# Performance work log

Hardware: AMD Instinct MI355X
Metric: run time of the kernel (lower is better)

The kernel has to match this reference:

```python
import jax, jax.numpy as jnp
import numpy as np

N = 10000   # nodes
E = 50000   # edges
G = 8       # graphs in batch
IN = 16     # input_dim
H = 64      # hidden_dim
EH = 32     # edge-network hidden
L = 3       # num ECC layers
BN_EPS = 1e-5


def _xavier(k, shape):
    fan_in, fan_out = shape[-2], shape[-1]
    s = jnp.sqrt(2.0 / (fan_in + fan_out)).astype(jnp.float32)
    return jax.random.normal(k, shape, jnp.float32) * s


def setup_inputs() -> dict:
    key = jax.random.key(0)
    ks = jax.random.split(key, 10)
    x = jax.random.normal(ks[0], (N, IN), jnp.float32)
    edge_index = jax.random.randint(ks[1], (2, E), 0, N, jnp.int32)
    batch = jnp.sort(jax.random.randint(ks[2], (N,), 0, G, jnp.int32))
    return {
        "x": x,
        "edge_index": edge_index,
        "batch": batch,
        "emb_w": _xavier(ks[3], (IN, H)),
        "emb_b": jnp.zeros((H,), jnp.float32),
        "e1_w": _xavier(ks[4], (L, 1, EH)),
        "e1_b": jnp.zeros((L, EH), jnp.float32),
        "e2_w": _xavier(ks[5], (L, EH, H * H)),
        "e2_b": jnp.zeros((L, H * H), jnp.float32),
        "self_w": _xavier(ks[6], (L, H, H)),
        "self_b": jnp.zeros((L, H), jnp.float32),
        "bn_g": jnp.ones((L, H), jnp.float32),
        "bn_b": jnp.zeros((L, H), jnp.float32),
        "cls_w": _xavier(ks[7], (2 * H, 1)),
        "cls_b": jnp.zeros((1,), jnp.float32),
    }


def reference(x, edge_index, batch, emb_w, emb_b, e1_w, e1_b, e2_w, e2_b,
              self_w, self_b, bn_g, bn_b, cls_w, cls_b):
    src, dst = edge_index[0], edge_index[1]
    # in-degree of targets for 'mean' aggregation (computed once; edge structure fixed)
    deg = jnp.clip(jax.ops.segment_sum(jnp.ones((E,), x.dtype), dst, num_segments=N), 1.0, None)

    h = x @ emb_w + emb_b  # [N, H] input embedding
    for l in range(L):
        # edge_attr: L2 distance between first 3 hidden channels of endpoints, [E,1]
        d = h[src, :3] - h[dst, :3]
        ea = jnp.sqrt(jnp.sum(d * d, axis=1, keepdims=True))
        # edge network -> per-edge dynamic weight matrix [E, H, H]
        hid = jax.nn.relu(ea @ e1_w[l] + e1_b[l])          # [E, EH]
        W = (hid @ e2_w[l] + e2_b[l]).reshape(E, H, H)
        # message: x_j (source features) times per-edge weight
        msg = jnp.einsum('ei,eio->eo', h[src], W)          # [E, H]
        agg = jax.ops.segment_sum(msg, dst, num_segments=N) / deg[:, None]
        h2 = agg + h @ self_w[l] + self_b[l]               # ECC output + self transform
        # BatchNorm1d (training-mode batch stats, biased variance), then ReLU
        mu = h2.mean(axis=0)
        var = h2.var(axis=0)
        h = jax.nn.relu(bn_g[l] * (h2 - mu) * jax.lax.rsqrt(var + BN_EPS) + bn_b[l])
        # dropout is a no-op in eval mode

    cnt = jnp.clip(jax.ops.segment_sum(jnp.ones((N,), h.dtype), batch, num_segments=G), 1.0, None)
    h_mean = jax.ops.segment_sum(h, batch, num_segments=G) / cnt[:, None]
    h_max = jax.ops.segment_max(h, batch, num_segments=G)
    h_pooled = jnp.concatenate([h_mean, h_max], axis=1)    # [G, 2H]
    return jax.nn.sigmoid(h_pooled @ cls_w + cls_b)        # [G, 1]
```

## Files before the change

### kernel.cpp

```cpp
#include <hip/hip_runtime.h>
#include <math.h>

#define N_NODES 10000
#define N_EDGES 50000
#define N_GRAPHS 8
#define IN_DIM  16
#define HID     64
#define EHID    32
#define NLAYER  3
#define NK      33
#define BN_EPS  1e-5f
#define POOL_BLOCKS 63
#define LAYER_BLOCKS 625
#define MAXDEG  64

#define FB_EMBED 2500
#define FB_S2    (16 * NK * NLAYER)
#define FB_AUX   3
#define FB_TOTAL (FB_EMBED + FB_S2 + FB_AUX)

#define OFF_H0     0u
#define OFF_H2A    640000u
#define OFF_H2B    1280000u
#define OFF_ATAB   1920000u
#define OFF_CTAB   2325504u
#define OFF_S      2731008u
#define OFF_NB     2731136u
#define OFF_CUR    2731200u
#define OFF_CSRC   2741200u
#define OFF_STATS  3381200u
#define OFF_GSUM   3381584u
#define OFF_GMAX   3382096u
#define OFF_GCNT   3382608u
#define OFF_CNTR   3382616u

__device__ __forceinline__ float rl(float v, int i) {
    return __int_as_float(__builtin_amdgcn_readlane(__float_as_int(v), i));
}

__device__ __forceinline__ void bn_coef(const float* __restrict__ sPrev,
                                        const float* __restrict__ gPrev,
                                        const float* __restrict__ bPrev,
                                        int c, float& sc, float& sf) {
    float mu  = sPrev[c] * (1.0f / N_NODES);
    float var = fmaf(-mu, mu, sPrev[64 + c] * (1.0f / N_NODES));
    float rstd = 1.0f / sqrtf(var + BN_EPS);
    sc = gPrev[c] * rstd;
    sf = fmaf(-sc, mu, bPrev[c]);
}

__device__ __forceinline__ int bp_list(const float* __restrict__ e1w,
                                       const float* __restrict__ e1b,
                                       int l, float* t) {
    int c = 0;
    for (int j = 0; j < EHID; ++j) {
        float a = e1w[l * EHID + j], b = e1b[l * EHID + j];
        if ((a > 0.f && b < 0.f) || (a < 0.f && b > 0.f)) t[c++] = -b / a;
    }
    for (int i = 1; i < c; ++i) {
        float v = t[i]; int j = i - 1;
        while (j >= 0 && t[j] > v) { t[j + 1] = t[j]; --j; }
        t[j + 1] = v;
    }
    return c;
}

__global__ void k_front(const float* __restrict__ x, const float* __restrict__ emb_w,
                        const float* __restrict__ emb_b,
                        const float* __restrict__ e1w, const float* __restrict__ e1b,
                        const float* __restrict__ e2w, const float* __restrict__ e2b,
                        float* __restrict__ s_arr, int* __restrict__ nb,
                        int* __restrict__ cur, float* __restrict__ stats,
                        float* __restrict__ gsum, float* __restrict__ gmax,
                        int* __restrict__ gcnt, int* __restrict__ counter,
                        float* __restrict__ Atab, float* __restrict__ Ctab,
                        float* __restrict__ h0) {
    int b = blockIdx.x, tid = threadIdx.x;
    if (b < FB_EMBED) {
        int idx = b * 256 + tid;
        int n = idx >> 6, o = idx & 63;
        const float* xr = x + n * IN_DIM;
        float acc = emb_b[o];
        #pragma unroll
        for (int i = 0; i < IN_DIM; ++i) acc = fmaf(xr[i], emb_w[i * HID + o], acc);
        h0[idx] = acc;
    } else if (b < FB_EMBED + FB_S2) {
        __shared__ float st[EHID];
        __shared__ int snb;
        __shared__ float sma[EHID], smb[EHID];
        __shared__ float4 rA[4][64], rC[4][64];
        int job = b - FB_EMBED;
        int qq  = job / (NK * NLAYER);
        int rem = job % (NK * NLAYER);
        int k = rem / NLAYER, l = rem % NLAYER;
        if (tid == 0) {
            float t[EHID];
            int c = bp_list(e1w, e1b, l, t);
            snb = c;
            for (int i = 0; i < c; ++i) st[i] = t[i];
        }
        __syncthreads();
        int nbl = snb;
        if (k > nbl) return;
        if (tid < EHID) {
            float a = e1w[l * EHID + tid], bb = e1b[l * EHID + tid];
            float lo = (k == 0) ? 0.f : st[k - 1];
            float hi = st[k];
            float p  = (k == nbl) ? (lo + 1.0f) : 0.5f * (lo + hi);
            float m  = (p * a + bb > 0.f) ? 1.f : 0.f;
            sma[tid] = m * a;
            smb[tid] = m * bb;
        }
        __syncthreads();
        int lane6 = tid & 63, grp = tid >> 6;
        int f4 = qq * 64 + lane6;
        const float4* w4 = (const float4*)e2w;
        float4 accA = make_float4(0.f, 0.f, 0.f, 0.f);
        float4 accC = make_float4(0.f, 0.f, 0.f, 0.f);
        #pragma unroll
        for (int jj = 0; jj < 8; ++jj) {
            int j = grp * 8 + jj;
            float4 w = w4[(l * EHID + j) * 1024 + f4];
            float ma = sma[j], mb = smb[j];
            accA.x = fmaf(ma, w.x, accA.x); accA.y = fmaf(ma, w.y, accA.y);
            accA.z = fmaf(ma, w.z, accA.z); accA.w = fmaf(ma, w.w, accA.w);
            accC.x = fmaf(mb, w.x, accC.x); accC.y = fmaf(mb, w.y, accC.y);
            accC.z = fmaf(mb, w.z, accC.z); accC.w = fmaf(mb, w.w, accC.w);
        }
        rA[grp][lane6] = accA;
        rC[grp][lane6] = accC;
        __syncthreads();
        if (grp == 0) {
            float4 a0 = rA[0][lane6], a1 = rA[1][lane6], a2 = rA[2][lane6], a3 = rA[3][lane6];
            float4 c0 = rC[0][lane6], c1 = rC[1][lane6], c2 = rC[2][lane6], c3 = rC[3][lane6];
            float4 eb = ((const float4*)(e2b + l * HID * HID))[f4];
            float4 A, C;
            A.x = a0.x + a1.x + a2.x + a3.x; A.y = a0.y + a1.y + a2.y + a3.y;
            A.z = a0.z + a1.z + a2.z + a3.z; A.w = a0.w + a1.w + a2.w + a3.w;
            C.x = c0.x + c1.x + c2.x + c3.x + eb.x; C.y = c0.y + c1.y + c2.y + c3.y + eb.y;
            C.z = c0.z + c1.z + c2.z + c3.z + eb.z; C.w = c0.w + c1.w + c2.w + c3.w + eb.w;
            ((float4*)(Atab + (l * NK + k) * (HID * HID)))[f4] = A;
            ((float4*)(Ctab + (l * NK + k) * (HID * HID)))[f4] = C;
        }
    } else {
        int a = b - FB_EMBED - FB_S2;
        if (a == 0) {
            for (int i = tid; i < N_NODES; i += 256) cur[i] = 0;
        } else if (a == 1) {
            for (int i = tid; i < N_GRAPHS * HID; i += 256) { gsum[i] = 0.f; gmax[i] = 0.f; }
            if (tid < N_GRAPHS) gcnt[tid] = 0;
            if (tid == 0) *counter = 0;
        } else {
            for (int i = tid; i < NLAYER * 128; i += 256) stats[i] = 0.f;
            if (tid < NLAYER) {
                float t[EHID];
                int c = bp_list(e1w, e1b, tid, t);
                nb[tid] = c;
                for (int i = 0; i < c; ++i) s_arr[tid * NK + i] = t[i];
            }
        }
    }
}

__global__ void k_fill(const int* __restrict__ ei, int* __restrict__ cur,
                       int* __restrict__ csrc) {
    int e = blockIdx.x * blockDim.x + threadIdx.x;
    if (e < N_EDGES) {
        int dst = ei[N_EDGES + e];
        int pos = atomicAdd(&cur[dst], 1);
        if (pos < MAXDEG) csrc[dst * MAXDEG + pos] = ei[e];
    }
}

__global__ void __launch_bounds__(256, 3)
k_layer(const float* __restrict__ hb, int useBN,
        const float* __restrict__ sPrev, const float* __restrict__ gPrev,
        const float* __restrict__ bPrev,
        const int* __restrict__ csrc, const int* __restrict__ deg,
        const float* __restrict__ Atab, const float* __restrict__ Ctab,
        const float* __restrict__ s_arr, const int* __restrict__ nbp, int l,
        const float* __restrict__ sw_l, const float* __restrict__ sb_l,
        float* __restrict__ h2out, float* __restrict__ statsOut) {
    __shared__ float smW[3 * HID * HID];
    __shared__ float sRed[2][4][HID];
    int tid = threadIdx.x, wid = tid >> 6, lane = tid & 63;
    int nb = nbp[l];
    const float* A0 = Atab + l * NK * HID * HID;
    const float* C0 = Ctab + l * NK * HID * HID;
    {
        float4* s4 = (float4*)smW;
        const float4* w4 = (const float4*)sw_l;
        const float4* a4 = (const float4*)A0;
        const float4* c4 = (const float4*)C0;
        #pragma unroll
        for (int p = 0; p < 4; ++p) {
            int j = p * 256 + tid;
            s4[j] = w4[j];
            s4[1024 + j] = a4[j];
            s4[2048 + j] = c4[j];
        }
    }
    __syncthreads();
    float sc = 0.f, sf = 0.f;
    if (useBN) bn_coef(sPrev, gPrev, bPrev, lane, sc, sf);
    float sbv = sb_l[lane];
    int nodeBase = blockIdx.x * 16 + wid * 4;

    float hvv[4], pp[4], qq[4], aggE[4];
    #pragma unroll
    for (int c = 0; c < 4; ++c) {
        int node = nodeBase + c;
        float hv = hb[node * HID + lane];
        if (useBN) hv = fmaxf(fmaf(sc, hv, sf), 0.f);
        hvv[c] = hv;
        float p = 0.f, q = 0.f, aggv = 0.f;
        int cnt = min(deg[node], MAXDEG);
        const int base = node * MAXDEG;
        if (nb == 0) {
            int j = 0;
            for (; j + 4 <= cnt; j += 4) {
                int s0 = csrc[base + j],     s1 = csrc[base + j + 1];
                int s2 = csrc[base + j + 2], s3 = csrc[base + j + 3];
                float g0 = hb[s0 * HID + lane];
                float g1 = hb[s1 * HID + lane];
                float g2 = hb[s2 * HID + lane];
                float g3 = hb[s3 * HID + lane];
                #pragma unroll
                for (int u = 0; u < 4; ++u) {
                    float hs = (u == 0) ? g0 : (u == 1) ? g1 : (u == 2) ? g2 : g3;
                    if (useBN) hs = fmaxf(fmaf(sc, hs, sf), 0.f);
                    float diff = hs - hv;
                    float d0 = rl(diff, 0), d1 = rl(diff, 1), d2 = rl(diff, 2);
                    float ea = sqrtf(fmaf(d0, d0, fmaf(d1, d1, d2 * d2)));
                    p = fmaf(ea, hs, p);
                    q += hs;
                }
            }
            for (; j < cnt; ++j) {
                int s = csrc[base + j];
                float hs = hb[s * HID + lane];
                if (useBN) hs = fmaxf(fmaf(sc, hs, sf), 0.f);
                float diff = hs - hv;
                float d0 = rl(diff, 0), d1 = rl(diff, 1), d2 = rl(diff, 2);
                float ea = sqrtf(fmaf(d0, d0, fmaf(d1, d1, d2 * d2)));
                p = fmaf(ea, hs, p);
                q += hs;
            }
        } else {
            for (int j = 0; j < cnt; ++j) {
                int src = csrc[base + j];
                float hs = hb[src * HID + lane];
                if (useBN) hs = fmaxf(fmaf(sc, hs, sf), 0.f);
                float diff = hs - hv;
                float d0 = rl(diff, 0), d1 = rl(diff, 1), d2 = rl(diff, 2);
                float ea = sqrtf(fmaf(d0, d0, fmaf(d1, d1, d2 * d2)));
                int k = 0;
                for (int i = 0; i < nb; ++i) k += (ea > s_arr[l * NK + i]) ? 1 : 0;
                const float* A = Atab + (l * NK + k) * (HID * HID);
                const float* C = Ctab + (l * NK + k) * (HID * HID);
                float au = 0.f, cu = 0.f;
                for (int i = 0; i < HID; ++i) {
                    float hi = rl(hs, i);
                    au = fmaf(hi, A[i * HID + lane], au);
                    cu = fmaf(hi, C[i * HID + lane], cu);
                }
                aggv += fmaf(ea, au, cu);
            }
        }
        pp[c] = p; qq[c] = q; aggE[c] = aggv;
    }

    float acc[4], agg[4];
    #pragma unroll
    for (int c = 0; c < 4; ++c) { acc[c] = sbv; agg[c] = 0.f; }
    #pragma unroll
    for (int i = 0; i < HID; ++i) {
        float ws = smW[i * HID + lane];
        float wa = smW[HID * HID + i * HID + lane];
        float wc = smW[2 * HID * HID + i * HID + lane];
        #pragma unroll
        for (int c = 0; c < 4; ++c) {
            acc[c] = fmaf(rl(hvv[c], i), ws, acc[c]);
            agg[c] = fmaf(rl(pp[c], i), wa, agg[c]);
            agg[c] = fmaf(rl(qq[c], i), wc, agg[c]);
        }
    }

    float ls = 0.f, ls2 = 0.f;
    #pragma unroll
    for (int c = 0; c < 4; ++c) {
        int node = nodeBase + c;
        float invd = 1.0f / fmaxf((float)deg[node], 1.0f);
        float v = fmaf(agg[c] + aggE[c], invd, acc[c]);
        h2out[node * HID + lane] = v;
        ls += v; ls2 = fmaf(v, v, ls2);
    }
    sRed[0][wid][lane] = ls;
    sRed[1][wid][lane] = ls2;
    __syncthreads();
    if (tid < HID) {
        float s  = sRed[0][0][tid] + sRed[0][1][tid] + sRed[0][2][tid] + sRed[0][3][tid];
        float s2 = sRed[1][0][tid] + sRed[1][1][tid] + sRed[1][2][tid] + sRed[1][3][tid];
        atomicAdd(&statsOut[tid], s);
        atomicAdd(&statsOut[64 + tid], s2);
    }
}

__global__ void k_bnpool(const float* __restrict__ h2cur, const float* __restrict__ s2,
                         const float* __restrict__ g2, const float* __restrict__ b2,
                         const int* __restrict__ batch,
                         float* __restrict__ gsum, float* __restrict__ gmax,
                         int* __restrict__ gcnt, int* __restrict__ counter,
                         const float* __restrict__ cw, const float* __restrict__ cb,
                         float* __restrict__ out) {
    int tid = threadIdx.x;
    int wid = (blockIdx.x * 256 + tid) >> 6, lane = tid & 63;
    float sc, sf; bn_coef(s2, g2, b2, lane, sc, sf);
    int n0 = wid * 40;
    int n1 = min(n0 + 40, N_NODES);
    float asum = 0.f, amax = 0.f;
    int cb2 = -1, run = 0;
    for (int n = n0; n < n1; ++n) {
        int b = batch[n];
        float v = fmaxf(fmaf(sc, h2cur[n * HID + lane], sf), 0.f);
        if (b != cb2) {
            if (cb2 >= 0) {
                atomicAdd(&gsum[cb2 * HID + lane], asum);
                atomicMax((int*)&gmax[cb2 * HID + lane], __float_as_int(amax));
                if (lane == 0) atomicAdd(&gcnt[cb2], run);
            }
            cb2 = b; asum = v; amax = v; run = 1;
        } else {
            asum += v; amax = fmaxf(amax, v); ++run;
        }
    }
    if (cb2 >= 0) {
        atomicAdd(&gsum[cb2 * HID + lane], asum);
        atomicMax((int*)&gmax[cb2 * HID + lane], __float_as_int(amax));
        if (lane == 0) atomicAdd(&gcnt[cb2], run);
    }
    __threadfence();
    __shared__ int lastFlag;
    if (tid == 0) {
        int old = __hip_atomic_fetch_add(counter, 1, __ATOMIC_ACQ_REL, __HIP_MEMORY_SCOPE_AGENT);
        lastFlag = (old == POOL_BLOCKS - 1);
    }
    __syncthreads();
    if (lastFlag && tid < N_GRAPHS) {
        int g = tid;
        float cnt = fmaxf((float)__hip_atomic_load(&gcnt[g], __ATOMIC_RELAXED, __HIP_MEMORY_SCOPE_AGENT), 1.f);
        float acc = cb[0];
        for (int o2 = 0; o2 < HID; ++o2) {
            float sv = __hip_atomic_load(&gsum[g * HID + o2], __ATOMIC_RELAXED, __HIP_MEMORY_SCOPE_AGENT);
            acc = fmaf(sv / cnt, cw[o2], acc);
        }
        for (int o2 = 0; o2 < HID; ++o2) {
            int iv = __hip_atomic_load((int*)&gmax[g * HID + o2], __ATOMIC_RELAXED, __HIP_MEMORY_SCOPE_AGENT);
            acc = fmaf(__int_as_float(iv), cw[HID + o2], acc);
        }
        out[g] = 1.0f / (1.0f + expf(-acc));
    }
}

extern "C" void kernel_launch(void* const* d_in, const int* in_sizes, int n_in,
                              void* d_out, int out_size, void* d_ws, size_t ws_size,
                              hipStream_t stream) {
    const float* x      = (const float*)d_in[0];
    const int*   ei     = (const int*)  d_in[1];
    const int*   batch  = (const int*)  d_in[2];
    const float* emb_w  = (const float*)d_in[3];
    const float* emb_b  = (const float*)d_in[4];
    const float* e1_w   = (const float*)d_in[5];
    const float* e1_b   = (const float*)d_in[6];
    const float* e2_w   = (const float*)d_in[7];
    const float* e2_b   = (const float*)d_in[8];
    const float* self_w = (const float*)d_in[9];
    const float* self_b = (const float*)d_in[10];
    const float* bn_g   = (const float*)d_in[11];
    const float* bn_b   = (const float*)d_in[12];
    const float* cls_w  = (const float*)d_in[13];
    const float* cls_b  = (const float*)d_in[14];
    float* outp = (float*)d_out;

    float* wsf = (float*)d_ws;
    float* h0     = wsf + OFF_H0;
    float* h2a    = wsf + OFF_H2A;
    float* h2b    = wsf + OFF_H2B;
    float* Atab   = wsf + OFF_ATAB;
    float* Ctab   = wsf + OFF_CTAB;
    float* s_arr  = wsf + OFF_S;
    int*   nb     = (int*)(wsf + OFF_NB);
    int*   cur    = (int*)(wsf + OFF_CUR);
    int*   csrc   = (int*)(wsf + OFF_CSRC);
    float* stats  = wsf + OFF_STATS;
    float* gsum   = wsf + OFF_GSUM;
    float* gmax   = wsf + OFF_GMAX;
    int*   gcnt   = (int*)(wsf + OFF_GCNT);
    int*   cntr   = (int*)(wsf + OFF_CNTR);

    k_front<<<FB_TOTAL, 256, 0, stream>>>(x, emb_w, emb_b, e1_w, e1_b, e2_w, e2_b,
                                          s_arr, nb, cur, stats, gsum, gmax, gcnt, cntr,
                                          Atab, Ctab, h0);
    k_fill<<<(N_EDGES + 255) / 256, 256, 0, stream>>>(ei, cur, csrc);

    for (int l = 0; l < NLAYER; ++l) {
        const float* hb    = (l == 0) ? h0 : ((l == 1) ? h2a : h2b);
        float*       h2out = (l == 1) ? h2b : h2a;
        const float* sPrev = stats + (l - 1) * 128;
        const float* gPrev = bn_g + (l - 1) * HID;
        const float* bPrev = bn_b + (l - 1) * HID;
        int useBN = (l > 0);
        k_layer<<<LAYER_BLOCKS, 256, 0, stream>>>(hb, useBN, sPrev, gPrev, bPrev,
                                                  csrc, cur,
                                                  Atab, Ctab, s_arr, nb, l,
                                                  self_w + l * HID * HID, self_b + l * HID,
                                                  h2out, stats + l * 128);
    }

    k_bnpool<<<POOL_BLOCKS, 256, 0, stream>>>(h2a, stats + 2 * 128, bn_g + 2 * HID, bn_b + 2 * HID,
                                              batch, gsum, gmax, gcnt, cntr, cls_w, cls_b, outp);
}
```

Baseline: 146.1 us.

## Fuse three layer kernels and pooling into one persistent kernel with grid barriers

Replaces the three per-layer launches and the separate BN/pool launch with a single kernel of 625 blocks that loops over layers and synchronizes through a software grid barrier built on an atomic counter. This removes three kernel launch boundaries and their drain/ramp gaps. It relies on all 625 blocks being co-resident (launch bounds of 3 blocks/CU with 48KB shared memory each); if they are not, the barrier deadlocks. Barrier spinning and the loss of hardware ordering add their own cost.

Result: slower. 404.9 us (+177.2%).

```diff
diff --git a/kernel.cpp b/kernel.cpp
--- a/kernel.cpp
+++ b/kernel.cpp
@@ -33,6 +33,7 @@
 #define OFF_GMAX   3382096u
 #define OFF_GCNT   3382608u
 #define OFF_CNTR   3382616u
+#define OFF_BAR    3382620u
 
 __device__ __forceinline__ float rl(float v, int i) {
     return __int_as_float(__builtin_amdgcn_readlane(__float_as_int(v), i));
@@ -65,6 +66,17 @@
     return c;
 }
 
+__device__ __forceinline__ void grid_bar(int* bar, int target) {
+    __syncthreads();
+    if (threadIdx.x == 0) {
+        __threadfence();
+        __hip_atomic_fetch_add(bar, 1, __ATOMIC_ACQ_REL, __HIP_MEMORY_SCOPE_AGENT);
+        while (__hip_atomic_load(bar, __ATOMIC_ACQUIRE, __HIP_MEMORY_SCOPE_AGENT) < target) { }
+        __threadfence();
+    }
+    __syncthreads();
+}
+
 __global__ void k_front(const float* __restrict__ x, const float* __restrict__ emb_w,
                         const float* __restrict__ emb_b,
                         const float* __restrict__ e1w, const float* __restrict__ e1b,
@@ -73,6 +85,7 @@
                         int* __restrict__ cur, float* __restrict__ stats,
                         float* __restrict__ gsum, float* __restrict__ gmax,
                         int* __restrict__ gcnt, int* __restrict__ counter,
+                        int* __restrict__ bar,
                         float* __restrict__ Atab, float* __restrict__ Ctab,
                         float* __restrict__ h0) {
     int b = blockIdx.x, tid = threadIdx.x;
@@ -149,7 +162,7 @@
         } else if (a == 1) {
             for (int i = tid; i < N_GRAPHS * HID; i += 256) { gsum[i] = 0.f; gmax[i] = 0.f; }
             if (tid < N_GRAPHS) gcnt[tid] = 0;
-            if (tid == 0) *counter = 0;
+            if (tid == 0) { *counter = 0; *bar = 0; }
         } else {
             for (int i = tid; i < NLAYER * 128; i += 256) stats[i] = 0.f;
             if (tid < NLAYER) {
@@ -173,192 +186,197 @@
 }
 
 __global__ void __launch_bounds__(256, 3)
-k_layer(const float* __restrict__ hb, int useBN,
-        const float* __restrict__ sPrev, const float* __restrict__ gPrev,
-        const float* __restrict__ bPrev,
-        const int* __restrict__ csrc, const int* __restrict__ deg,
-        const float* __restrict__ Atab, const float* __restrict__ Ctab,
-        const float* __restrict__ s_arr, const int* __restrict__ nbp, int l,
-        const float* __restrict__ sw_l, const float* __restrict__ sb_l,
-        float* __restrict__ h2out, float* __restrict__ statsOut) {
+k_layers(float* __restrict__ h0, float* __restrict__ h2a, float* __restrict__ h2b,
+         const int* __restrict__ csrc, const int* __restrict__ deg,
+         const float* __restrict__ Atab, const float* __restrict__ Ctab,
+         const float* __restrict__ s_arr, const int* __restrict__ nbp,
+         const float* __restrict__ self_w, const float* __restrict__ self_b,
+         const float* __restrict__ bn_g, const float* __restrict__ bn_b,
+         const int* __restrict__ batch,
+         float* __restrict__ stats, float* __restrict__ gsum, float* __restrict__ gmax,
+         int* __restrict__ gcnt, int* __restrict__ counter, int* __restrict__ bar,
+         const float* __restrict__ cls_w, const float* __restrict__ cls_b,
+         float* __restrict__ out) {
     __shared__ float smW[3 * HID * HID];
     __shared__ float sRed[2][4][HID];
     int tid = threadIdx.x, wid = tid >> 6, lane = tid & 63;
-    int nb = nbp[l];
-    const float* A0 = Atab + l * NK * HID * HID;
-    const float* C0 = Ctab + l * NK * HID * HID;
-    {
-        float4* s4 = (float4*)smW;
-        const float4* w4 = (const float4*)sw_l;
-        const float4* a4 = (const float4*)A0;
-        const float4* c4 = (const float4*)C0;
-        #pragma unroll
-        for (int p = 0; p < 4; ++p) {
-            int j = p * 256 + tid;
-            s4[j] = w4[j];
-            s4[1024 + j] = a4[j];
-            s4[2048 + j] = c4[j];
-        }
-    }
-    __syncthreads();
-    float sc = 0.f, sf = 0.f;
-    if (useBN) bn_coef(sPrev, gPrev, bPrev, lane, sc, sf);
-    float sbv = sb_l[lane];
     int nodeBase = blockIdx.x * 16 + wid * 4;
 
-    float hvv[4], pp[4], qq[4], aggE[4];
-    #pragma unroll
-    for (int c = 0; c < 4; ++c) {
-        int node = nodeBase + c;
-        float hv = hb[node * HID + lane];
-        if (useBN) hv = fmaxf(fmaf(sc, hv, sf), 0.f);
-        hvv[c] = hv;
-        float p = 0.f, q = 0.f, aggv = 0.f;
-        int cnt = min(deg[node], MAXDEG);
-        const int base = node * MAXDEG;
-        if (nb == 0) {
-            int j = 0;
-            for (; j + 4 <= cnt; j += 4) {
-                int s0 = csrc[base + j],     s1 = csrc[base + j + 1];
-                int s2 = csrc[base + j + 2], s3 = csrc[base + j + 3];
-                float g0 = hb[s0 * HID + lane];
-                float g1 = hb[s1 * HID + lane];
-                float g2 = hb[s2 * HID + lane];
-                float g3 = hb[s3 * HID + lane];
-                #pragma unroll
-                for (int u = 0; u < 4; ++u) {
-                    float hs = (u == 0) ? g0 : (u == 1) ? g1 : (u == 2) ? g2 : g3;
-                    if (useBN) hs = fmaxf(fmaf(sc, hs, sf), 0.f);
-                    float diff = hs - hv;
+    for (int l = 0; l < NLAYER; ++l) {
+        const float* hb    = (l == 0) ? h0 : ((l == 1) ? h2a : h2b);
+        float*       h2out = (l == 1) ? h2b : h2a;
+        int nb = nbp[l];
+        const float* A0 = Atab + l * NK * HID * HID;
+        const float* C0 = Ctab + l * NK * HID * HID;
+        const float* sw_l = self_w + l * HID * HID;
+        {
+            float4* s4 = (float4*)smW;
+            const float4* w4 = (const float4*)sw_l;
+            const float4* a4 = (const float4*)A0;
+            const float4* c4 = (const float4*)C0;
+            #pragma unroll
+            for (int p = 0; p < 4; ++p) {
+                int j = p * 256 + tid;
+                s4[j] = w4[j];
+                s4[1024 + j] = a4[j];
+                s4[2048 + j] = c4[j];
+            }
+        }
+        __syncthreads();
+        float sc = 0.f, sf = 0.f;
+        if (l > 0) bn_coef(stats + (l - 1) * 128, bn_g + (l - 1) * HID,
+                           bn_b + (l - 1) * HID, lane, sc, sf);
+        float sbv = self_b[l * HID + lane];
+
+        float hvv[4], pp[4], qq[4], aggE[4];
+        #pragma unroll
+        for (int c = 0; c < 4; ++c) {
+            int node = nodeBase + c;
+            float hv = hb[node * HID + lane];
+            if (l > 0) hv = fmaxf(fmaf(sc, hv, sf), 0.f);
+            hvv[c] = hv;
+            float p = 0.f, q = 0.f, aggv = 0.f;
+            int cnt = min(deg[node], MAXDEG);
+            const int base = node * MAXDEG;
+            if (nb == 0) {
+                int j = 0;
+                for (; j + 4 <= cnt; j += 4) {
+                    int s0 = csrc[base + j],     s1 = csrc[base + j + 1];
+                    int s2 = csrc[base + j + 2], s3 = csrc[base + j + 3];
+                    float g0 = hb[s0 * HID + lane];
+                    float g1 = hb[s1 * HID + lane];
+                    float g2 = hb[s2 * HID + lane];
+                    float g3 = hb[s3 * HID + lane];
+                    #pragma unroll
+                    for (int u = 0; u < 4; ++u) {
+                        float hs = (u == 0) ? g0 : (u == 1) ? g1 : (u == 2) ? g2 : g3;
+                        if (l > 0) hs = fmaxf(fmaf(sc, hs, sf), 0.f);
+                        float diff = hs - hvv[c];
+                        float d0 = rl(diff, 0), d1 = rl(diff, 1), d2 = rl(diff, 2);
+                        float ea = sqrtf(fmaf(d0, d0, fmaf(d1, d1, d2 * d2)));
+                        p = fmaf(ea, hs, p);
+                        q += hs;
+                    }
+                }
+                for (; j < cnt; ++j) {
+                    int s = csrc[base + j];
+                    float hs = hb[s * HID + lane];
+                    if (l > 0) hs = fmaxf(fmaf(sc, hs, sf), 0.f);
+                    float diff = hs - hvv[c];
                     float d0 = rl(diff, 0), d1 = rl(diff, 1), d2 = rl(diff, 2);
                     float ea = sqrtf(fmaf(d0, d0, fmaf(d1, d1, d2 * d2)));
                     p = fmaf(ea, hs, p);
                     q += hs;
                 }
-            }
-            for (; j < cnt; ++j) {
-                int s = csrc[base + j];
-                float hs = hb[s * HID + lane];
-                if (useBN) hs = fmaxf(fmaf(sc, hs, sf), 0.f);
-                float diff = hs - hv;
-                float d0 = rl(diff, 0), d1 = rl(diff, 1), d2 = rl(diff, 2);
-                float ea = sqrtf(fmaf(d0, d0, fmaf(d1, d1, d2 * d2)));
-                p = fmaf(ea, hs, p);
-                q += hs;
-            }
-        } else {
-            for (int j = 0; j < cnt; ++j) {
-                int src = csrc[base + j];
-                float hs = hb[src * HID + lane];
-                if (useBN) hs = fmaxf(fmaf(sc, hs, sf), 0.f);
-                float diff = hs - hv;
-                float d0 = rl(diff, 0), d1 = rl(diff, 1), d2 = rl(diff, 2);
-                float ea = sqrtf(fmaf(d0, d0, fmaf(d1, d1, d2 * d2)));
-                int k = 0;
-                for (int i = 0; i < nb; ++i) k += (ea > s_arr[l * NK + i]) ? 1 : 0;
-                const float* A = Atab + (l * NK + k) * (HID * HID);
-                const float* C = Ctab + (l * NK + k) * (HID * HID);
-                float au = 0.f, cu = 0.f;
-                for (int i = 0; i < HID; ++i) {
-                    float hi = rl(hs, i);
-                    au = fmaf(hi, A[i * HID + lane], au);
-                    cu = fmaf(hi, C[i * HID + lane], cu);
+            } else {
+                for (int j = 0; j < cnt; ++j) {
+                    int src = csrc[base + j];
+                    float hs = hb[src * HID + lane];
+                    if (l > 0) hs = fmaxf(fmaf(sc, hs, sf), 0.f);
+                    float diff = hs - hvv[c];
+                    float d0 = rl(diff, 0), d1 = rl(diff, 1), d2 = rl(diff, 2);
+                    float ea = sqrtf(fmaf(d0, d0, fmaf(d1, d1, d2 * d2)));
+                    int k = 0;
+                    for (int i = 0; i < nb; ++i) k += (ea > s_arr[l * NK + i]) ? 1 : 0;
+                    const float* A = Atab + (l * NK + k) * (HID * HID);
+                    const float* C = Ctab + (l * NK + k) * (HID * HID);
+                    float au = 0.f, cu = 0.f;
+                    for (int i = 0; i < HID; ++i) {
+                        float hi = rl(hs, i);
+                        au = fmaf(hi, A[i * HID + lane], au);
+                        cu = fmaf(hi, C[i * HID + lane], cu);
+                    }
+                    aggv += fmaf(ea, au, cu);
                 }
-                aggv += fmaf(ea, au, cu);
-            }
-        }
-        pp[c] = p; qq[c] = q; aggE[c] = aggv;
-    }
-
-    float acc[4], agg[4];
-    #pragma unroll
-    for (int c = 0; c < 4; ++c) { acc[c] = sbv; agg[c] = 0.f; }
-    #pragma unroll
-    for (int i = 0; i < HID; ++i) {
-        float ws = smW[i * HID + lane];
-        float wa = smW[HID * HID + i * HID + lane];
-        float wc = smW[2 * HID * HID + i * HID + lane];
+            }
+            pp[c] = p; qq[c] = q; aggE[c] = aggv;
+        }
+
+        float acc[4], agg[4];
+        #pragma unroll
+        for (int c = 0; c < 4; ++c) { acc[c] = sbv; agg[c] = 0.f; }
+        #pragma unroll
+        for (int i = 0; i < HID; ++i) {
+            float ws = smW[i * HID + lane];
+            float wa = smW[HID * HID + i * HID + lane];
+            float wc = smW[2 * HID * HID + i * HID + lane];
+            #pragma unroll
+            for (int c = 0; c < 4; ++c) {
+                acc[c] = fmaf(rl(hvv[c], i), ws, acc[c]);
+                agg[c] = fmaf(rl(pp[c], i), wa, agg[c]);
+                agg[c] = fmaf(rl(qq[c], i), wc, agg[c]);
+            }
+        }
+
+        float ls = 0.f, ls2 = 0.f;
         #pragma unroll
         for (int c = 0; c < 4; ++c) {
-            acc[c] = fmaf(rl(hvv[c], i), ws, acc[c]);
-            agg[c] = fmaf(rl(pp[c], i), wa, agg[c]);
-            agg[c] = fmaf(rl(qq[c], i), wc, agg[c]);
-        }
-    }
-
-    float ls = 0.f, ls2 = 0.f;
-    #pragma unroll
-    for (int c = 0; c < 4; ++c) {
-        int node = nodeBase + c;
-        float invd = 1.0f / fmaxf((float)deg[node], 1.0f);
-        float v = fmaf(agg[c] + aggE[c], invd, acc[c]);
-        h2out[node * HID + lane] = v;
-        ls += v; ls2 = fmaf(v, v, ls2);
-    }
-    sRed[0][wid][lane] = ls;
-    sRed[1][wid][lane] = ls2;
-    __syncthreads();
-    if (tid < HID) {
-        float s  = sRed[0][0][tid] + sRed[0][1][tid] + sRed[0][2][tid] + sRed[0][3][tid];
-        float s2 = sRed[1][0][tid] + sRed[1][1][tid] + sRed[1][2][tid] + sRed[1][3][tid];
-        atomicAdd(&statsOut[tid], s);
-        atomicAdd(&statsOut[64 + tid], s2);
-    }
-}
-
-__global__ void k_bnpool(const float* __restrict__ h2cur, const float* __restrict__ s2,
-                         const float* __restrict__ g2, const float* __restrict__ b2,
-                         const int* __restrict__ batch,
-                         float* __restrict__ gsum, float* __restrict__ gmax,
-                         int* __restrict__ gcnt, int* __restrict__ counter,
-                         const float* __restrict__ cw, const float* __restrict__ cb,
-                         float* __restrict__ out) {
-    int tid = threadIdx.x;
-    int wid = (blockIdx.x * 256 + tid) >> 6, lane = tid & 63;
-    float sc, sf; bn_coef(s2, g2, b2, lane, sc, sf);
-    int n0 = wid * 40;
-    int n1 = min(n0 + 40, N_NODES);
-    float asum = 0.f, amax = 0.f;
-    int cb2 = -1, run = 0;
-    for (int n = n0; n < n1; ++n) {
-        int b = batch[n];
-        float v = fmaxf(fmaf(sc, h2cur[n * HID + lane], sf), 0.f);
-        if (b != cb2) {
-            if (cb2 >= 0) {
-                atomicAdd(&gsum[cb2 * HID + lane], asum);
-                atomicMax((int*)&gmax[cb2 * HID + lane], __float_as_int(amax));
-                if (lane == 0) atomicAdd(&gcnt[cb2], run);
-            }
-            cb2 = b; asum = v; amax = v; run = 1;
-        } else {
-            asum += v; amax = fmaxf(amax, v); ++run;
-        }
-    }
-    if (cb2 >= 0) {
-        atomicAdd(&gsum[cb2 * HID + lane], asum);
-        atomicMax((int*)&gmax[cb2 * HID + lane], __float_as_int(amax));
-        if (lane == 0) atomicAdd(&gcnt[cb2], run);
-    }
-    __threadfence();
-    __shared__ int lastFlag;
-    if (tid == 0) {
-        int old = __hip_atomic_fetch_add(counter, 1, __ATOMIC_ACQ_REL, __HIP_MEMORY_SCOPE_AGENT);
-        lastFlag = (old == POOL_BLOCKS - 1);
-    }
-    __syncthreads();
-    if (lastFlag && tid < N_GRAPHS) {
-        int g = tid;
-        float cnt = fmaxf((float)__hip_atomic_load(&gcnt[g], __ATOMIC_RELAXED, __HIP_MEMORY_SCOPE_AGENT), 1.f);
-        float acc = cb[0];
-        for (int o2 = 0; o2 < HID; ++o2) {
-            float sv = __hip_atomic_load(&gsum[g * HID + o2], __ATOMIC_RELAXED, __HIP_MEMORY_SCOPE_AGENT);
-            acc = fmaf(sv / cnt, cw[o2], acc);
-        }
-        for (int o2 = 0; o2 < HID; ++o2) {
-            int iv = __hip_atomic_load((int*)&gmax[g * HID + o2], __ATOMIC_RELAXED, __HIP_MEMORY_SCOPE_AGENT);
-            acc = fmaf(__int_as_float(iv), cw[HID + o2], acc);
-        }
-        out[g] = 1.0f / (1.0f + expf(-acc));
+            int node = nodeBase + c;
+            float invd = 1.0f / fmaxf((float)deg[node], 1.0f);
+            float v = fmaf(agg[c] + aggE[c], invd, acc[c]);
+            h2out[node * HID + lane] = v;
+            ls += v; ls2 = fmaf(v, v, ls2);
+        }
+        __syncthreads();
+        sRed[0][wid][lane] = ls;
+        sRed[1][wid][lane] = ls2;
+        __syncthreads();
+        if (tid < HID) {
+            float s  = sRed[0][0][tid] + sRed[0][1][tid] + sRed[0][2][tid] + sRed[0][3][tid];
+            float s2 = sRed[1][0][tid] + sRed[1][1][tid] + sRed[1][2][tid] + sRed[1][3][tid];
+            atomicAdd(&stats[l * 128 + tid], s);
+            atomicAdd(&stats[l * 128 + 64 + tid], s2);
+        }
+        grid_bar(bar, (l + 1) * LAYER_BLOCKS);
+    }
+
+    if (blockIdx.x < POOL_BLOCKS) {
+        float sc, sf; bn_coef(stats + 2 * 128, bn_g + 2 * HID, bn_b + 2 * HID, lane, sc, sf);
+        int w = (blockIdx.x * 256 + tid) >> 6;
+        int n0 = w * 40;
+        int n1 = min(n0 + 40, N_NODES);
+        float asum = 0.f, amax = 0.f;
+        int cb2 = -1, run = 0;
+        for (int n = n0; n < n1; ++n) {
+            int b = batch[n];
+            float v = fmaxf(fmaf(sc, h2a[n * HID + lane], sf), 0.f);
+            if (b != cb2) {
+                if (cb2 >= 0) {
+                    atomicAdd(&gsum[cb2 * HID + lane], asum);
+                    atomicMax((int*)&gmax[cb2 * HID + lane], __float_as_int(amax));
+                    if (lane == 0) atomicAdd(&gcnt[cb2], run);
+                }
+                cb2 = b; asum = v; amax = v; run = 1;
+            } else {
+                asum += v; amax = fmaxf(amax, v); ++run;
+            }
+        }
+        if (cb2 >= 0) {
+            atomicAdd(&gsum[cb2 * HID + lane], asum);
+            atomicMax((int*)&gmax[cb2 * HID + lane], __float_as_int(amax));
+            if (lane == 0) atomicAdd(&gcnt[cb2], run);
+        }
+        __threadfence();
+        __shared__ int lastFlag;
+        if (tid == 0) {
+            int old = __hip_atomic_fetch_add(counter, 1, __ATOMIC_ACQ_REL, __HIP_MEMORY_SCOPE_AGENT);
+            lastFlag = (old == POOL_BLOCKS - 1);
+        }
+        __syncthreads();
+        if (lastFlag && tid < N_GRAPHS) {
+            int g = tid;
+            float cnt = fmaxf((float)__hip_atomic_load(&gcnt[g], __ATOMIC_RELAXED, __HIP_MEMORY_SCOPE_AGENT), 1.f);
+            float acc = cls_b[0];
+            for (int o2 = 0; o2 < HID; ++o2) {
+                float sv = __hip_atomic_load(&gsum[g * HID + o2], __ATOMIC_RELAXED, __HIP_MEMORY_SCOPE_AGENT);
+                acc = fmaf(sv / cnt, cls_w[o2], acc);
+            }
+            for (int o2 = 0; o2 < HID; ++o2) {
+                int iv = __hip_atomic_load((int*)&gmax[g * HID + o2], __ATOMIC_RELAXED, __HIP_MEMORY_SCOPE_AGENT);
+                acc = fmaf(__int_as_float(iv), cls_w[HID + o2], acc);
+            }
+            out[g] = 1.0f / (1.0f + expf(-acc));
+        }
     }
 }
 
@@ -397,26 +415,15 @@
     float* gmax   = wsf + OFF_GMAX;
     int*   gcnt   = (int*)(wsf + OFF_GCNT);
     int*   cntr   = (int*)(wsf + OFF_CNTR);
+    int*   bar    = (int*)(wsf + OFF_BAR);
 
     k_front<<<FB_TOTAL, 256, 0, stream>>>(x, emb_w, emb_b, e1_w, e1_b, e2_w, e2_b,
-                                          s_arr, nb, cur, stats, gsum, gmax, gcnt, cntr,
+                                          s_arr, nb, cur, stats, gsum, gmax, gcnt, cntr, bar,
                                           Atab, Ctab, h0);
     k_fill<<<(N_EDGES + 255) / 256, 256, 0, stream>>>(ei, cur, csrc);
-
-    for (int l = 0; l < NLAYER; ++l) {
-        const float* hb    = (l == 0) ? h0 : ((l == 1) ? h2a : h2b);
-        float*       h2out = (l == 1) ? h2b : h2a;
-        const float* sPrev = stats + (l - 1) * 128;
-        const float* gPrev = bn_g + (l - 1) * HID;
-        const float* bPrev = bn_b + (l - 1) * HID;
-        int useBN = (l > 0);
-        k_layer<<<LAYER_BLOCKS, 256, 0, stream>>>(hb, useBN, sPrev, gPrev, bPrev,
-                                                  csrc, cur,
-                                                  Atab, Ctab, s_arr, nb, l,
-                                                  self_w + l * HID * HID, self_b + l * HID,
-                                                  h2out, stats + l * 128);
-    }
-
-    k_bnpool<<<POOL_BLOCKS, 256, 0, stream>>>(h2a, stats + 2 * 128, bn_g + 2 * HID, bn_b + 2 * HID,
-                                              batch, gsum, gmax, gcnt, cntr, cls_w, cls_b, outp);
-}
+    k_layers<<<LAYER_BLOCKS, 256, 0, stream>>>(h0, h2a, h2b, csrc, cur,
+                                               Atab, Ctab, s_arr, nb,
+                                               self_w, self_b, bn_g, bn_b, batch,
+                                               stats, gsum, gmax, gcnt, cntr, bar,
+                                               cls_w, cls_b, outp);
+}
```
